# Kernel optimization log

Hardware: AMD Instinct MI355X
Metric: run time of the kernel (lower is better)

The kernel has to match this reference:

```python
import jax, jax.numpy as jnp
import numpy as np

DIM = 768
NUM_HEADS = 12
POLY_DEG = 3
GRID = (24, 24)
BATCH = 16


def _make_powers():
    H, W = GRID
    ii, jj = np.meshgrid(np.arange(H), np.arange(W), indexing='ij')
    coords = np.stack([ii.ravel(), jj.ravel()], axis=-1).astype(np.float32)  # [HW, 2]
    dists = np.abs(coords[:, None, :] - coords[None, :, :]).sum(-1)  # L1 cdist [HW, HW]
    powers = np.stack([dists ** i for i in range(POLY_DEG + 1)], axis=0)  # [deg+1, HW, HW]
    return jnp.asarray(powers, dtype=jnp.float32)


def setup_inputs() -> dict:
    key = jax.random.key(0)
    ks = jax.random.split(key, 5)
    N = GRID[0] * GRID[1] + 1  # 577
    x = jax.random.normal(ks[0], (BATCH, N, DIM), dtype=jnp.float32)
    # nn.Linear weights stored as [in, out] for direct matmul; qkv_bias=False
    W_qkv = jax.random.normal(ks[1], (DIM, 3 * DIM), dtype=jnp.float32) * (DIM ** -0.5)
    W_proj = jax.random.normal(ks[2], (DIM, DIM), dtype=jnp.float32) * (DIM ** -0.5)
    b_proj = jnp.zeros((DIM,), dtype=jnp.float32)
    # small scale keeps polynomial bias (distances up to 46, cubed) numerically sane
    poly_coeffs = jax.random.normal(ks[3], (NUM_HEADS, POLY_DEG + 1), dtype=jnp.float32) * 0.01
    powers = _make_powers()
    return {"x": x, "W_qkv": W_qkv, "W_proj": W_proj, "b_proj": b_proj,
            "poly_coeffs": poly_coeffs, "powers": powers}


def reference(x, W_qkv, W_proj, b_proj, poly_coeffs, powers):
    B, N, C = x.shape
    h = NUM_HEADS
    d = C // h
    scale = d ** -0.5
    qkv = (x @ W_qkv).reshape(B, N, 3, h, d)
    qkv = jnp.transpose(qkv, (2, 0, 3, 1, 4))  # [3, B, h, N, d]
    q, k, v = qkv[0], qkv[1], qkv[2]
    # polynomial relative-position bias, padded with zeros for CLS row/col
    rpe = jnp.einsum('hd,dxy->hxy', poly_coeffs, powers)  # [h, HW, HW]
    rpe = jnp.pad(rpe, ((0, 0), (1, 0), (1, 0)))  # [h, N, N]
    attn = scale * jnp.einsum('bhnd,bhmd->bhnm', q, k) + rpe[None]
    attn = jax.nn.softmax(attn, axis=-1)
    out = jnp.einsum('bhnm,bhmd->bhnd', attn, v)
    out = jnp.transpose(out, (0, 2, 1, 3)).reshape(B, N, C)
    return out @ W_proj + b_proj
```

## Files before the change

kernel.cpp:

```cpp
#include <hip/hip_runtime.h>


using u16 = unsigned short;
using u32 = unsigned int;

typedef __bf16 bf16x8 __attribute__((ext_vector_type(8)));
typedef float f32x4 __attribute__((ext_vector_type(4)));

__device__ inline u16 f2bf(float f) {
    u32 u = __builtin_bit_cast(u32, f);
    u32 r = u + 0x7fffu + ((u >> 16) & 1u);
    return (u16)(r >> 16);
}
__device__ inline float bf2f(u16 x) {
    return __builtin_bit_cast(float, (u32)x << 16);
}

__device__ inline f32x4 mfma16(bf16x8 a, bf16x8 b, f32x4 c) {
    return __builtin_amdgcn_mfma_f32_16x16x32_bf16(a, b, c, 0, 0, 0);
}

__device__ inline float fexp2(float x) { return __builtin_amdgcn_exp2f(x); }

__device__ inline int xcd_remap(int bid, int nwg) {
    const int q = nwg >> 3, r = nwg & 7;
    const int xcd = bid & 7, idx = bid >> 3;
    return (xcd < r ? xcd * (q + 1) : r * (q + 1) + (xcd - r) * q) + idx;
}

__device__ inline float dpp_max16(float v) {
    int x;
    x = __builtin_amdgcn_update_dpp(0, __builtin_bit_cast(int, v), 0xB1, 0xF, 0xF, true);
    v = fmaxf(v, __builtin_bit_cast(float, x));
    x = __builtin_amdgcn_update_dpp(0, __builtin_bit_cast(int, v), 0x4E, 0xF, 0xF, true);
    v = fmaxf(v, __builtin_bit_cast(float, x));
    x = __builtin_amdgcn_update_dpp(0, __builtin_bit_cast(int, v), 0x124, 0xF, 0xF, true);
    v = fmaxf(v, __builtin_bit_cast(float, x));
    x = __builtin_amdgcn_update_dpp(0, __builtin_bit_cast(int, v), 0x128, 0xF, 0xF, true);
    v = fmaxf(v, __builtin_bit_cast(float, x));
    return v;
}
__device__ inline float dpp_sum16(float v) {
    int x;
    x = __builtin_amdgcn_update_dpp(0, __builtin_bit_cast(int, v), 0xB1, 0xF, 0xF, true);
    v += __builtin_bit_cast(float, x);
    x = __builtin_amdgcn_update_dpp(0, __builtin_bit_cast(int, v), 0x4E, 0xF, 0xF, true);
    v += __builtin_bit_cast(float, x);
    x = __builtin_amdgcn_update_dpp(0, __builtin_bit_cast(int, v), 0x124, 0xF, 0xF, true);
    v += __builtin_bit_cast(float, x);
    x = __builtin_amdgcn_update_dpp(0, __builtin_bit_cast(int, v), 0x128, 0xF, 0xF, true);
    v += __builtin_bit_cast(float, x);
    return v;
}

#define GLOAD_LDS16(g, l)                                                          \
    __builtin_amdgcn_global_load_lds((const __attribute__((address_space(1))) u32*)(g), \
                                     (__attribute__((address_space(3))) u32*)(l), 16, 0, 0)

#define BAR()    asm volatile("s_barrier" ::: "memory")
#define WAITV8() asm volatile("s_waitcnt vmcnt(8)" ::: "memory")
#define WAITV4() asm volatile("s_waitcnt vmcnt(4)" ::: "memory")
#define WAITV0() asm volatile("s_waitcnt vmcnt(0)" ::: "memory")

__global__ void k_prep(const float* __restrict__ x, const float* __restrict__ Wq,
                       const float* __restrict__ Wp, u16* __restrict__ xb,
                       u16* __restrict__ wqkv, u16* __restrict__ wprj) {
    const int bid = blockIdx.x;
    const int t = threadIdx.x;
    if (bid < 576) {
        __shared__ float tile[64][65];
        const float* src;
        u16* dst;
        int C, rt, ct;
        if (bid < 432) { src = Wq; dst = wqkv; C = 2304; rt = bid / 36; ct = bid % 36; }
        else { const int b2 = bid - 432; src = Wp; dst = wprj; C = 768; rt = b2 / 12; ct = b2 % 12; }
        const int row0 = rt * 64, col0 = ct * 64;
#pragma unroll
        for (int it = 0; it < 4; ++it) {
            const int row = it * 16 + (t >> 4);
            const float4 v = *(const float4*)&src[(size_t)(row0 + row) * C + col0 + (t & 15) * 4];
            tile[row][(t & 15) * 4 + 0] = v.x;
            tile[row][(t & 15) * 4 + 1] = v.y;
            tile[row][(t & 15) * 4 + 2] = v.z;
            tile[row][(t & 15) * 4 + 3] = v.w;
        }
        __syncthreads();
#pragma unroll
        for (int it = 0; it < 4; ++it) {
            const int oc = it * 16 + (t >> 4);
            const int orr = (t & 15) * 4;
            ushort4 o;
            o.x = f2bf(tile[orr + 0][oc]);
            o.y = f2bf(tile[orr + 1][oc]);
            o.z = f2bf(tile[orr + 2][oc]);
            o.w = f2bf(tile[orr + 3][oc]);
            *(ushort4*)&dst[(size_t)(col0 + oc) * 768 + row0 + orr] = o;
        }
    } else {
        const int n4 = 9232 * 768 / 4;
        const int stride = (2048 - 576) * 256;
        for (int i = (bid - 576) * 256 + t; i < n4; i += stride) {
            float4 v = ((const float4*)x)[i];
            ushort4 o;
            o.x = f2bf(v.x); o.y = f2bf(v.y); o.z = f2bf(v.z); o.w = f2bf(v.w);
            ((ushort4*)xb)[i] = o;
        }
    }
}

__device__ inline void stageAB(const u16* __restrict__ Ag, const u16* __restrict__ Bg,
                               u16* L, int t) {
#pragma unroll
    for (int c = 0; c < 2; ++c) {
        const int p = c * 256 + t;
        const int row = p >> 2, ch = p & 3;
        const int src = row * 768 + ((ch ^ ((row >> 1) & 3)) * 8);
        GLOAD_LDS16(Ag + src, L + p * 8);
        GLOAD_LDS16(Bg + src, L + 4096 + p * 8);
    }
}
__device__ inline bf16x8 ldfrag32(const u16* base, int row, int slot) {
    return *(const bf16x8*)(base + row * 32 + ((slot ^ ((row >> 1) & 3)) * 8));
}

template <int MODE, int NB>
__launch_bounds__(256, 2)
__global__ void k_gemm(const u16* __restrict__ A, const u16* __restrict__ Bw,
                       u16* __restrict__ q_out, u16* __restrict__ k_out,
                       u16* __restrict__ v_out,
                       float* __restrict__ f_out, const float* __restrict__ bias) {
    constexpr int NT = 24;
    constexpr int M = 9232;
    const int wgid = xcd_remap(blockIdx.x, gridDim.x);
    const int mbase = (wgid / NB) * 128;
    const int nbase = (wgid - (wgid / NB) * NB) * 128;
    __shared__ alignas(16) u16 lds[4][8192];
    const int t = threadIdx.x;
    const int lane = t & 63, w = t >> 6;
    const int lr = lane & 15, lg = lane >> 4;
    const int wrow = (w >> 1) * 64, wcol = (w & 1) * 64;
    const u16* Ag = A + (size_t)mbase * 768;
    const u16* Bg = Bw + (size_t)nbase * 768;
    f32x4 acc[4][4] = {};

    stageAB(Ag, Bg, &lds[0][0], t);
    stageAB(Ag + 32, Bg + 32, &lds[1][0], t);
    stageAB(Ag + 64, Bg + 64, &lds[2][0], t);
    WAITV8();
    BAR();

    for (int kt = 0; kt < NT; ++kt) {
        const u16* Lc = &lds[kt & 3][0];
        if (kt + 3 < NT)
            stageAB(Ag + (kt + 3) * 32, Bg + (kt + 3) * 32, &lds[(kt + 3) & 3][0], t);
        bf16x8 af[4], bv[4];
#pragma unroll
        for (int i = 0; i < 4; ++i)
            af[i] = ldfrag32(Lc, wrow + i * 16 + lr, lg);
#pragma unroll
        for (int j = 0; j < 4; ++j)
            bv[j] = ldfrag32(Lc + 4096, wcol + j * 16 + lr, lg);
        __builtin_amdgcn_s_setprio(1);
#pragma unroll
        for (int i = 0; i < 4; ++i)
#pragma unroll
            for (int j = 0; j < 4; ++j)
                acc[i][j] = mfma16(af[i], bv[j], acc[i][j]);
        __builtin_amdgcn_s_setprio(0);
        if (kt + 1 < NT) {
            if (kt < NT - 3)       { WAITV8(); }
            else if (kt == NT - 3) { WAITV4(); }
            else                   { WAITV0(); }
            BAR();
        }
    }

#pragma unroll
    for (int i = 0; i < 4; ++i) {
#pragma unroll
        for (int j = 0; j < 4; ++j) {
            const int col = nbase + wcol + j * 16 + lr;
#pragma unroll
            for (int r = 0; r < 4; ++r) {
                const int row = mbase + wrow + i * 16 + 4 * lg + r;
                if (row < M) {
                    if (MODE == 0) {
                        const int bb = row / 577;
                        const int nn = row - bb * 577;
                        const int tt = col / 768;
                        const int rem = col - tt * 768;
                        const int hh = rem >> 6, dd = rem & 63;
                        const size_t bh = (size_t)bb * 12 + hh;
                        const u16 val = f2bf(acc[i][j][r]);
                        if (tt == 0)      q_out[(bh * 640 + nn) * 64 + dd] = val;
                        else if (tt == 1) k_out[(bh * 640 + nn) * 64 + dd] = val;
                        else              v_out[(bh * 64 + dd) * 640 + nn] = val;
                    } else {
                        f_out[(size_t)row * 768 + col] = acc[i][j][r] + bias[col];
                    }
                }
            }
        }
    }
}

__launch_bounds__(256, 2)
__global__ void k_attn(const u16* __restrict__ Qg, const u16* __restrict__ Kg,
                       const u16* __restrict__ Vtg, const float* __restrict__ coef,
                       u16* __restrict__ Og) {
    const int wgid = xcd_remap(blockIdx.x, gridDim.x);
    const int bh = wgid / 5;
    const int qt = wgid - bh * 5;
    const int b = bh / 12, h = bh - b * 12;
    const int t = threadIdx.x;
    const int lane = t & 63, w = t >> 6;
    const int lr = lane & 15, lg = lane >> 4;
    __shared__ alignas(16) u16 Kl[2][4096];
    __shared__ alignas(16) u16 Vl[2][4096];

    const float l2e = 1.4426950408889634f;
    const float hc0 = coef[h * 4 + 0] * l2e, hc1 = coef[h * 4 + 1] * l2e,
                hc2 = coef[h * 4 + 2] * l2e, hc3 = coef[h * 4 + 3] * l2e;

    const int qrow0 = qt * 128 + w * 32;
    bf16x8 qa[2][2];
#pragma unroll
    for (int i = 0; i < 2; ++i) {
        const u16* qp = Qg + ((size_t)bh * 640 + qrow0 + i * 16 + lr) * 64;
        qa[i][0] = *(const bf16x8*)(qp + lg * 8);
        qa[i][1] = *(const bf16x8*)(qp + 32 + lg * 8);
    }

    float gi[2][4], gj[2][4], nvf[2][4];
#pragma unroll
    for (int i = 0; i < 2; ++i)
#pragma unroll
        for (int r = 0; r < 4; ++r) {
            const int n = qrow0 + i * 16 + 4 * lg + r;
            nvf[i][r] = (n == 0) ? 0.f : 1.f;
            const int nm1 = (n > 0) ? n - 1 : 0;
            const int qi = nm1 / 24;
            gi[i][r] = (float)qi;
            gj[i][r] = (float)(nm1 - qi * 24);
        }

    float M[2][4], L[2][4];
#pragma unroll
    for (int i = 0; i < 2; ++i)
#pragma unroll
        for (int r = 0; r < 4; ++r) { M[i][r] = -3e38f; L[i][r] = 0.f; }
    f32x4 acco[2][4] = {};
    const float scale2 = 0.125f * 1.4426950408889634f;
    const int ch0 = ((lg ^ (lr & 7))) * 8;

    const u16* Ksb = Kg + (size_t)bh * 640 * 64;
    const u16* Vsb = Vtg + (size_t)bh * 64 * 640;
    const int sr0 = lane >> 3, sc = lane & 7;
    const int kr0 = 16 * w + sr0, kr1 = kr0 + 8;
    const int kd0 = kr0 * 64 + ((sc ^ (kr0 & 7)) * 8);
    const int kd1 = kr1 * 64 + ((sc ^ (kr1 & 7)) * 8);

    {
        uint4 k0 = *(const uint4*)(Ksb + kr0 * 64 + sc * 8);
        uint4 k1 = *(const uint4*)(Ksb + kr1 * 64 + sc * 8);
        uint4 v0 = *(const uint4*)(Vsb + (size_t)kr0 * 640 + sc * 8);
        uint4 v1 = *(const uint4*)(Vsb + (size_t)kr1 * 640 + sc * 8);
        *(uint4*)(&Kl[0][kd0]) = k0;
        *(uint4*)(&Kl[0][kd1]) = k1;
        *(uint4*)(&Vl[0][kd0]) = v0;
        *(uint4*)(&Vl[0][kd1]) = v1;
    }
    __syncthreads();
    int cur = 0;

    for (int kt = 0; kt < 9; ++kt) {
        const u16* Kc = &Kl[cur][0];
        const u16* Vc = &Vl[cur][0];
        u16* pb0 = &Kl[cur ^ 1][16 * w * 64];
        u16* pb1 = &Vl[cur ^ 1][16 * w * 64];

        f32x4 sac[2][4];
        __builtin_amdgcn_s_setprio(1);
#pragma unroll
        for (int cb = 0; cb < 4; ++cb) {
            const int row = cb * 16 + lr;
            const bf16x8 kb0 = *(const bf16x8*)(Kc + row * 64 + ch0);
            const bf16x8 kb1 = *(const bf16x8*)(Kc + row * 64 + (ch0 ^ 32));
#pragma unroll
            for (int i = 0; i < 2; ++i) {
                f32x4 z = {};
                z = mfma16(qa[i][0], kb0, z);
                sac[i][cb] = mfma16(qa[i][1], kb1, z);
            }
        }
        __builtin_amdgcn_s_setprio(0);

        float tm[2][4];
#pragma unroll
        for (int i = 0; i < 2; ++i)
#pragma unroll
            for (int r = 0; r < 4; ++r) tm[i][r] = -3e38f;
#pragma unroll
        for (int cb = 0; cb < 4; ++cb) {
            const int m = kt * 64 + cb * 16 + lr;
            const float mvf = (m == 0) ? 0.f : 1.f;
            const int mm1 = (m > 0) ? m - 1 : 0;
            const int pi = mm1 / 24;
            const float ci = (float)pi;
            const float cj = (float)(mm1 - pi * 24);
#pragma unroll
            for (int i = 0; i < 2; ++i)
#pragma unroll
                for (int r = 0; r < 4; ++r) {
                    const float d = fabsf(gi[i][r] - ci) + fabsf(gj[i][r] - cj);
                    float rp = fmaf(hc3, d, hc2);
                    rp = fmaf(rp, d, hc1);
                    rp = fmaf(rp, d, hc0);
                    const float v = fmaf(sac[i][cb][r], scale2,
                                         rp * (mvf * nvf[i][r]));
                    sac[i][cb][r] = v;
                    tm[i][r] = fmaxf(tm[i][r], v);
                }
        }
#pragma unroll
        for (int i = 0; i < 2; ++i)
#pragma unroll
            for (int r = 0; r < 4; ++r) tm[i][r] = dpp_max16(tm[i][r]);

        float over = -3e38f;
#pragma unroll
        for (int i = 0; i < 2; ++i)
#pragma unroll
            for (int r = 0; r < 4; ++r) over = fmaxf(over, tm[i][r] - M[i][r]);
        if (__any(over > 11.5f)) {
#pragma unroll
            for (int i = 0; i < 2; ++i)
#pragma unroll
                for (int r = 0; r < 4; ++r) {
                    const float Mn = fmaxf(M[i][r], tm[i][r]);
                    const float a = fexp2(M[i][r] - Mn);
                    L[i][r] *= a;
                    acco[i][0][r] *= a; acco[i][1][r] *= a;
                    acco[i][2][r] *= a; acco[i][3][r] *= a;
                    M[i][r] = Mn;
                }
        }

#pragma unroll
        for (int i = 0; i < 2; ++i) {
            u16* pb = i ? pb1 : pb0;
#pragma unroll
            for (int cb = 0; cb < 4; ++cb)
#pragma unroll
                for (int r = 0; r < 4; ++r) {
                    const float p = fexp2(sac[i][cb][r] - M[i][r]);
                    L[i][r] += p;
                    const int rw = 4 * lg + r;
                    pb[rw * 64 + (((2 * cb + (lr >> 3)) ^ (rw & 7)) * 8) + (lr & 7)] = f2bf(p);
                }
        }

        uint4 nk0, nk1, nv0, nv1;
        {
            const u16* Ks = Ksb + (size_t)(kt + 1) * 64 * 64;
            const u16* Vs = Vsb + (size_t)(kt + 1) * 64;
            nk0 = *(const uint4*)(Ks + kr0 * 64 + sc * 8);
            nk1 = *(const uint4*)(Ks + kr1 * 64 + sc * 8);
            nv0 = *(const uint4*)(Vs + (size_t)kr0 * 640 + sc * 8);
            nv1 = *(const uint4*)(Vs + (size_t)kr1 * 640 + sc * 8);
        }

        const bf16x8 pa00 = *(const bf16x8*)(pb0 + lr * 64 + ch0);
        const bf16x8 pa01 = *(const bf16x8*)(pb0 + lr * 64 + (ch0 ^ 32));
        const bf16x8 pa10 = *(const bf16x8*)(pb1 + lr * 64 + ch0);
        const bf16x8 pa11 = *(const bf16x8*)(pb1 + lr * 64 + (ch0 ^ 32));
        __builtin_amdgcn_s_setprio(1);
#pragma unroll
        for (int f = 0; f < 4; ++f) {
            const int vrow = f * 16 + lr;
            const bf16x8 vb0 = *(const bf16x8*)(Vc + vrow * 64 + ch0);
            const bf16x8 vb1 = *(const bf16x8*)(Vc + vrow * 64 + (ch0 ^ 32));
            acco[0][f] = mfma16(pa00, vb0, acco[0][f]);
            acco[0][f] = mfma16(pa01, vb1, acco[0][f]);
            acco[1][f] = mfma16(pa10, vb0, acco[1][f]);
            acco[1][f] = mfma16(pa11, vb1, acco[1][f]);
        }
        __builtin_amdgcn_s_setprio(0);

        *(uint4*)(&Kl[cur ^ 1][kd0]) = nk0;
        *(uint4*)(&Kl[cur ^ 1][kd1]) = nk1;
        *(uint4*)(&Vl[cur ^ 1][kd0]) = nv0;
        *(uint4*)(&Vl[cur ^ 1][kd1]) = nv1;
        __syncthreads();
        cur ^= 1;
    }

    {
        const u16* Kc = &Kl[cur][0];
        const u16* Vc = &Vl[cur][0];
        u16* pb0 = &Kl[cur ^ 1][16 * w * 64];
        u16* pb1 = &Vl[cur ^ 1][16 * w * 64];
        const bf16x8 kb0 = *(const bf16x8*)(Kc + lr * 64 + ch0);
        const bf16x8 kb1 = *(const bf16x8*)(Kc + lr * 64 + (ch0 ^ 32));
        float s0[2][4], tm[2][4];
#pragma unroll
        for (int i = 0; i < 2; ++i) {
            f32x4 z = {};
            z = mfma16(qa[i][0], kb0, z);
            const f32x4 sc0 = mfma16(qa[i][1], kb1, z);
#pragma unroll
            for (int r = 0; r < 4; ++r) {
                const float d = fabsf(gi[i][r] - 23.f) + fabsf(gj[i][r] - 23.f);
                float rp = fmaf(hc3, d, hc2);
                rp = fmaf(rp, d, hc1);
                rp = fmaf(rp, d, hc0);
                float v = fmaf(sc0[r], scale2, rp * nvf[i][r]);
                v = (lr == 0) ? v : -1e30f;
                s0[i][r] = v;
                tm[i][r] = dpp_max16(v);
            }
        }
        float over = -3e38f;
#pragma unroll
        for (int i = 0; i < 2; ++i)
#pragma unroll
            for (int r = 0; r < 4; ++r) over = fmaxf(over, tm[i][r] - M[i][r]);
        if (__any(over > 11.5f)) {
#pragma unroll
            for (int i = 0; i < 2; ++i)
#pragma unroll
                for (int r = 0; r < 4; ++r) {
                    const float Mn = fmaxf(M[i][r], tm[i][r]);
                    const float a = fexp2(M[i][r] - Mn);
                    L[i][r] *= a;
                    acco[i][0][r] *= a; acco[i][1][r] *= a;
                    acco[i][2][r] *= a; acco[i][3][r] *= a;
                    M[i][r] = Mn;
                }
        }
#pragma unroll
        for (int i = 0; i < 2; ++i) {
            u16* pb = i ? pb1 : pb0;
#pragma unroll
            for (int cb = 0; cb < 4; ++cb)
#pragma unroll
                for (int r = 0; r < 4; ++r) {
                    const float p = (cb == 0) ? fexp2(s0[i][r] - M[i][r]) : 0.f;
                    L[i][r] += p;
                    const int rw = 4 * lg + r;
                    pb[rw * 64 + (((2 * cb + (lr >> 3)) ^ (rw & 7)) * 8) + (lr & 7)] = f2bf(p);
                }
        }
        const bf16x8 pa00 = *(const bf16x8*)(pb0 + lr * 64 + ch0);
        const bf16x8 pa10 = *(const bf16x8*)(pb1 + lr * 64 + ch0);
#pragma unroll
        for (int f = 0; f < 4; ++f) {
            const int vrow = f * 16 + lr;
            const bf16x8 vb0 = *(const bf16x8*)(Vc + vrow * 64 + ch0);
            acco[0][f] = mfma16(pa00, vb0, acco[0][f]);
            acco[1][f] = mfma16(pa10, vb0, acco[1][f]);
        }
    }

#pragma unroll
    for (int i = 0; i < 2; ++i)
#pragma unroll
        for (int r = 0; r < 4; ++r) {
            const float inv = __builtin_amdgcn_rcpf(dpp_sum16(L[i][r]));
            const int n = qrow0 + i * 16 + 4 * lg + r;
            if (n < 577) {
#pragma unroll
                for (int f = 0; f < 4; ++f)
                    Og[((size_t)b * 577 + n) * 768 + h * 64 + f * 16 + lr] =
                        f2bf(acco[i][f][r] * inv);
            }
        }
}

extern "C" void kernel_launch(void* const* d_in, const int* in_sizes, int n_in,
                              void* d_out, int out_size, void* d_ws, size_t ws_size,
                              hipStream_t stream) {
    const float* x      = (const float*)d_in[0];
    const float* W_qkv  = (const float*)d_in[1];
    const float* W_proj = (const float*)d_in[2];
    const float* b_proj = (const float*)d_in[3];
    const float* coef   = (const float*)d_in[4];
    float* out = (float*)d_out;
    char* ws = (char*)d_ws;

    u16* xb   = (u16*)(ws + 0);
    u16* Og   = (u16*)(ws + 0);
    u16* wqkv = (u16*)(ws + 14180352);
    u16* wprj = (u16*)(ws + 17719296);
    u16* Qg   = (u16*)(ws + 18898944);
    u16* Kg   = (u16*)(ws + 34627584);
    u16* Vtg  = (u16*)(ws + 50356224);

    k_prep<<<2048, 256, 0, stream>>>(x, W_qkv, W_proj, xb, wqkv, wprj);

    k_gemm<0, 18><<<18 * 73, 256, 0, stream>>>(xb, wqkv, Qg, Kg, Vtg,
                                               nullptr, nullptr);
    k_attn<<<960, 256, 0, stream>>>(Qg, Kg, Vtg, coef, Og);
    k_gemm<1, 6><<<6 * 73, 256, 0, stream>>>(Og, wprj, nullptr, nullptr,
                                             nullptr, out, b_proj);
}
```

Measured before the change: 166.3 us.

## Widen GEMM N-tile to 192 and switch to triple-buffered LDS pipeline

The GEMM tile width along N becomes a template parameter: both the QKV and output projections now use 128x192 tiles, with each wave covering 96 columns. The LDS ring drops from four stages with prefetch distance 3 to three stages with prefetch distance 2, and the vmcnt waits are adjusted to match. The wider tile cuts the number of workgroups and the redundant reloads of A, which raises data reuse. In exchange it uses more accumulator registers per wave and hides less global-load latency with the shallower prefetch.

```diff
diff --git a/kernel.cpp b/kernel.cpp
--- a/kernel.cpp
+++ b/kernel.cpp
@@ -58,8 +58,7 @@
                                      (__attribute__((address_space(3))) u32*)(l), 16, 0, 0)
 
 #define BAR()    asm volatile("s_barrier" ::: "memory")
-#define WAITV8() asm volatile("s_waitcnt vmcnt(8)" ::: "memory")
-#define WAITV4() asm volatile("s_waitcnt vmcnt(4)" ::: "memory")
+#define WAITV5() asm volatile("s_waitcnt vmcnt(5)" ::: "memory")
 #define WAITV0() asm volatile("s_waitcnt vmcnt(0)" ::: "memory")
 
 __global__ void k_prep(const float* __restrict__ x, const float* __restrict__ Wq,
@@ -108,22 +107,28 @@
     }
 }
 
+template <int NJ>
 __device__ inline void stageAB(const u16* __restrict__ Ag, const u16* __restrict__ Bg,
                                u16* L, int t) {
 #pragma unroll
     for (int c = 0; c < 2; ++c) {
         const int p = c * 256 + t;
         const int row = p >> 2, ch = p & 3;
-        const int src = row * 768 + ((ch ^ ((row >> 1) & 3)) * 8);
-        GLOAD_LDS16(Ag + src, L + p * 8);
-        GLOAD_LDS16(Bg + src, L + 4096 + p * 8);
+        GLOAD_LDS16(Ag + row * 768 + ((ch ^ ((row >> 1) & 3)) * 8), L + p * 8);
+    }
+#pragma unroll
+    for (int c = 0; c < NJ / 2; ++c) {
+        const int p = c * 256 + t;
+        const int row = p >> 2, ch = p & 3;
+        GLOAD_LDS16(Bg + row * 768 + ((ch ^ ((row >> 1) & 3)) * 8),
+                    L + 4096 + p * 8);
     }
 }
 __device__ inline bf16x8 ldfrag32(const u16* base, int row, int slot) {
     return *(const bf16x8*)(base + row * 32 + ((slot ^ ((row >> 1) & 3)) * 8));
 }
 
-template <int MODE, int NB>
+template <int MODE, int NB, int NJ>
 __launch_bounds__(256, 2)
 __global__ void k_gemm(const u16* __restrict__ A, const u16* __restrict__ Bw,
                        u16* __restrict__ q_out, u16* __restrict__ k_out,
@@ -131,46 +136,46 @@
                        float* __restrict__ f_out, const float* __restrict__ bias) {
     constexpr int NT = 24;
     constexpr int M = 9232;
+    constexpr int BN = NJ * 32;
     const int wgid = xcd_remap(blockIdx.x, gridDim.x);
     const int mbase = (wgid / NB) * 128;
-    const int nbase = (wgid - (wgid / NB) * NB) * 128;
-    __shared__ alignas(16) u16 lds[4][8192];
+    const int nbase = (wgid - (wgid / NB) * NB) * BN;
+    __shared__ alignas(16) u16 lds[3][4096 + NJ * 1024];
     const int t = threadIdx.x;
     const int lane = t & 63, w = t >> 6;
     const int lr = lane & 15, lg = lane >> 4;
-    const int wrow = (w >> 1) * 64, wcol = (w & 1) * 64;
+    const int wrow = (w >> 1) * 64, wcol = (w & 1) * (NJ * 16);
     const u16* Ag = A + (size_t)mbase * 768;
     const u16* Bg = Bw + (size_t)nbase * 768;
-    f32x4 acc[4][4] = {};
-
-    stageAB(Ag, Bg, &lds[0][0], t);
-    stageAB(Ag + 32, Bg + 32, &lds[1][0], t);
-    stageAB(Ag + 64, Bg + 64, &lds[2][0], t);
-    WAITV8();
+    f32x4 acc[4][NJ] = {};
+
+    stageAB<NJ>(Ag, Bg, &lds[0][0], t);
+    stageAB<NJ>(Ag + 32, Bg + 32, &lds[1][0], t);
+    WAITV5();
     BAR();
 
     for (int kt = 0; kt < NT; ++kt) {
-        const u16* Lc = &lds[kt & 3][0];
-        if (kt + 3 < NT)
-            stageAB(Ag + (kt + 3) * 32, Bg + (kt + 3) * 32, &lds[(kt + 3) & 3][0], t);
-        bf16x8 af[4], bv[4];
+        const u16* Lc = &lds[kt % 3][0];
+        const bool m2 = (kt + 2) < NT;
+        if (m2)
+            stageAB<NJ>(Ag + (kt + 2) * 32, Bg + (kt + 2) * 32,
+                        &lds[(kt + 2) % 3][0], t);
+        bf16x8 af[4], bv[NJ];
 #pragma unroll
         for (int i = 0; i < 4; ++i)
             af[i] = ldfrag32(Lc, wrow + i * 16 + lr, lg);
 #pragma unroll
-        for (int j = 0; j < 4; ++j)
+        for (int j = 0; j < NJ; ++j)
             bv[j] = ldfrag32(Lc + 4096, wcol + j * 16 + lr, lg);
         __builtin_amdgcn_s_setprio(1);
 #pragma unroll
         for (int i = 0; i < 4; ++i)
 #pragma unroll
-            for (int j = 0; j < 4; ++j)
+            for (int j = 0; j < NJ; ++j)
                 acc[i][j] = mfma16(af[i], bv[j], acc[i][j]);
         __builtin_amdgcn_s_setprio(0);
         if (kt + 1 < NT) {
-            if (kt < NT - 3)       { WAITV8(); }
-            else if (kt == NT - 3) { WAITV4(); }
-            else                   { WAITV0(); }
+            if (m2) { WAITV5(); } else { WAITV0(); }
             BAR();
         }
     }
@@ -178,7 +183,7 @@
 #pragma unroll
     for (int i = 0; i < 4; ++i) {
 #pragma unroll
-        for (int j = 0; j < 4; ++j) {
+        for (int j = 0; j < NJ; ++j) {
             const int col = nbase + wcol + j * 16 + lr;
 #pragma unroll
             for (int r = 0; r < 4; ++r) {
@@ -498,9 +503,9 @@
 
     k_prep<<<2048, 256, 0, stream>>>(x, W_qkv, W_proj, xb, wqkv, wprj);
 
-    k_gemm<0, 18><<<18 * 73, 256, 0, stream>>>(xb, wqkv, Qg, Kg, Vtg,
-                                               nullptr, nullptr);
+    k_gemm<0, 12, 6><<<12 * 73, 256, 0, stream>>>(xb, wqkv, Qg, Kg, Vtg,
+                                                  nullptr, nullptr);
     k_attn<<<960, 256, 0, stream>>>(Qg, Kg, Vtg, coef, Og);
-    k_gemm<1, 6><<<6 * 73, 256, 0, stream>>>(Og, wprj, nullptr, nullptr,
-                                             nullptr, out, b_proj);
-}
+    k_gemm<1, 4, 6><<<4 * 73, 256, 0, stream>>>(Og, wprj, nullptr, nullptr,
+                                                nullptr, out, b_proj);
+}
```

Result: slower. 172.9 us (+4.0%).

## Double attention KV tile width to 128 keys per iteration

Applied to the files above, without the earlier changes.

Switches the flash-attention loop from 64-key tiles (9 full iterations plus a tail) to 128-key tiles (4 full iterations plus an 80-key tail). The goal is fewer loop trips and barriers, with more MFMA and exp work between synchronizations. To support this, the K/V loading layout, the LDS swizzle (16-chunk XOR for V and the P buffer) and the P·V inner loop are restructured. LDS usage doubles to 64KB, which may limit occupancy against the 2-block launch bound, and register pressure grows with sac[2][8].

```diff
diff --git a/kernel.cpp b/kernel.cpp
--- a/kernel.cpp
+++ b/kernel.cpp
@@ -215,8 +215,8 @@
     const int t = threadIdx.x;
     const int lane = t & 63, w = t >> 6;
     const int lr = lane & 15, lg = lane >> 4;
-    __shared__ alignas(16) u16 Kl[2][4096];
-    __shared__ alignas(16) u16 Vl[2][4096];
+    __shared__ alignas(16) u16 Kl[2][8192];
+    __shared__ alignas(16) u16 Vl[2][8192];
 
     const float l2e = 1.4426950408889634f;
     const float hc0 = coef[h * 4 + 0] * l2e, hc1 = coef[h * 4 + 1] * l2e,
@@ -255,34 +255,31 @@
 
     const u16* Ksb = Kg + (size_t)bh * 640 * 64;
     const u16* Vsb = Vtg + (size_t)bh * 64 * 640;
-    const int sr0 = lane >> 3, sc = lane & 7;
-    const int kr0 = 16 * w + sr0, kr1 = kr0 + 8;
-    const int kd0 = kr0 * 64 + ((sc ^ (kr0 & 7)) * 8);
-    const int kd1 = kr1 * 64 + ((sc ^ (kr1 & 7)) * 8);
+    const int krow = 32 * w + (lane >> 1), kch0 = (lane & 1) * 4;
+    const int vrow = 16 * w + (lane >> 2), vch0 = (lane & 3) * 4;
 
     {
-        uint4 k0 = *(const uint4*)(Ksb + kr0 * 64 + sc * 8);
-        uint4 k1 = *(const uint4*)(Ksb + kr1 * 64 + sc * 8);
-        uint4 v0 = *(const uint4*)(Vsb + (size_t)kr0 * 640 + sc * 8);
-        uint4 v1 = *(const uint4*)(Vsb + (size_t)kr1 * 640 + sc * 8);
-        *(uint4*)(&Kl[0][kd0]) = k0;
-        *(uint4*)(&Kl[0][kd1]) = k1;
-        *(uint4*)(&Vl[0][kd0]) = v0;
-        *(uint4*)(&Vl[0][kd1]) = v1;
+#pragma unroll
+        for (int q = 0; q < 4; ++q) {
+            uint4 kv = *(const uint4*)(Ksb + (size_t)krow * 64 + (kch0 + q) * 8);
+            *(uint4*)(&Kl[0][krow * 64 + (((kch0 + q) ^ (krow & 7)) * 8)]) = kv;
+            uint4 vv = *(const uint4*)(Vsb + (size_t)vrow * 640 + (vch0 + q) * 8);
+            *(uint4*)(&Vl[0][vrow * 128 + (((vch0 + q) ^ (vrow & 15)) * 8)]) = vv;
+        }
     }
     __syncthreads();
     int cur = 0;
 
-    for (int kt = 0; kt < 9; ++kt) {
+    for (int kt = 0; kt < 4; ++kt) {
         const u16* Kc = &Kl[cur][0];
         const u16* Vc = &Vl[cur][0];
-        u16* pb0 = &Kl[cur ^ 1][16 * w * 64];
-        u16* pb1 = &Vl[cur ^ 1][16 * w * 64];
-
-        f32x4 sac[2][4];
+        u16* pb0 = &Kl[cur ^ 1][32 * w * 64];
+        u16* pb1 = &Vl[cur ^ 1][16 * w * 128];
+
+        f32x4 sac[2][8];
         __builtin_amdgcn_s_setprio(1);
 #pragma unroll
-        for (int cb = 0; cb < 4; ++cb) {
+        for (int cb = 0; cb < 8; ++cb) {
             const int row = cb * 16 + lr;
             const bf16x8 kb0 = *(const bf16x8*)(Kc + row * 64 + ch0);
             const bf16x8 kb1 = *(const bf16x8*)(Kc + row * 64 + (ch0 ^ 32));
@@ -301,8 +298,8 @@
 #pragma unroll
             for (int r = 0; r < 4; ++r) tm[i][r] = -3e38f;
 #pragma unroll
-        for (int cb = 0; cb < 4; ++cb) {
-            const int m = kt * 64 + cb * 16 + lr;
+        for (int cb = 0; cb < 8; ++cb) {
+            const int m = kt * 128 + cb * 16 + lr;
             const float mvf = (m == 0) ? 0.f : 1.f;
             const int mm1 = (m > 0) ? m - 1 : 0;
             const int pi = mm1 / 24;
@@ -350,47 +347,47 @@
         for (int i = 0; i < 2; ++i) {
             u16* pb = i ? pb1 : pb0;
 #pragma unroll
-            for (int cb = 0; cb < 4; ++cb)
+            for (int cb = 0; cb < 8; ++cb)
 #pragma unroll
                 for (int r = 0; r < 4; ++r) {
                     const float p = fexp2(sac[i][cb][r] - M[i][r]);
                     L[i][r] += p;
                     const int rw = 4 * lg + r;
-                    pb[rw * 64 + (((2 * cb + (lr >> 3)) ^ (rw & 7)) * 8) + (lr & 7)] = f2bf(p);
-                }
-        }
-
-        uint4 nk0, nk1, nv0, nv1;
+                    pb[rw * 128 + (((2 * cb + (lr >> 3)) ^ (rw & 15)) * 8) + (lr & 7)] = f2bf(p);
+                }
+        }
+
+        uint4 nk[4], nv[4];
         {
-            const u16* Ks = Ksb + (size_t)(kt + 1) * 64 * 64;
-            const u16* Vs = Vsb + (size_t)(kt + 1) * 64;
-            nk0 = *(const uint4*)(Ks + kr0 * 64 + sc * 8);
-            nk1 = *(const uint4*)(Ks + kr1 * 64 + sc * 8);
-            nv0 = *(const uint4*)(Vs + (size_t)kr0 * 640 + sc * 8);
-            nv1 = *(const uint4*)(Vs + (size_t)kr1 * 640 + sc * 8);
-        }
-
-        const bf16x8 pa00 = *(const bf16x8*)(pb0 + lr * 64 + ch0);
-        const bf16x8 pa01 = *(const bf16x8*)(pb0 + lr * 64 + (ch0 ^ 32));
-        const bf16x8 pa10 = *(const bf16x8*)(pb1 + lr * 64 + ch0);
-        const bf16x8 pa11 = *(const bf16x8*)(pb1 + lr * 64 + (ch0 ^ 32));
+            const u16* Ks = Ksb + (size_t)(kt + 1) * 128 * 64;
+            const u16* Vs = Vsb + (size_t)(kt + 1) * 128;
+#pragma unroll
+            for (int q = 0; q < 4; ++q) {
+                nk[q] = *(const uint4*)(Ks + (size_t)krow * 64 + (kch0 + q) * 8);
+                nv[q] = *(const uint4*)(Vs + (size_t)vrow * 640 + (vch0 + q) * 8);
+            }
+        }
+
         __builtin_amdgcn_s_setprio(1);
 #pragma unroll
-        for (int f = 0; f < 4; ++f) {
-            const int vrow = f * 16 + lr;
-            const bf16x8 vb0 = *(const bf16x8*)(Vc + vrow * 64 + ch0);
-            const bf16x8 vb1 = *(const bf16x8*)(Vc + vrow * 64 + (ch0 ^ 32));
-            acco[0][f] = mfma16(pa00, vb0, acco[0][f]);
-            acco[0][f] = mfma16(pa01, vb1, acco[0][f]);
-            acco[1][f] = mfma16(pa10, vb0, acco[1][f]);
-            acco[1][f] = mfma16(pa11, vb1, acco[1][f]);
+        for (int s = 0; s < 4; ++s) {
+            const bf16x8 pa0 = *(const bf16x8*)(pb0 + lr * 128 + (((4 * s + lg) ^ (lr & 15)) * 8));
+            const bf16x8 pa1 = *(const bf16x8*)(pb1 + lr * 128 + (((4 * s + lg) ^ (lr & 15)) * 8));
+#pragma unroll
+            for (int f = 0; f < 4; ++f) {
+                const int vr = f * 16 + lr;
+                const bf16x8 vb = *(const bf16x8*)(Vc + vr * 128 + (((4 * s + lg) ^ (vr & 15)) * 8));
+                acco[0][f] = mfma16(pa0, vb, acco[0][f]);
+                acco[1][f] = mfma16(pa1, vb, acco[1][f]);
+            }
         }
         __builtin_amdgcn_s_setprio(0);
 
-        *(uint4*)(&Kl[cur ^ 1][kd0]) = nk0;
-        *(uint4*)(&Kl[cur ^ 1][kd1]) = nk1;
-        *(uint4*)(&Vl[cur ^ 1][kd0]) = nv0;
-        *(uint4*)(&Vl[cur ^ 1][kd1]) = nv1;
+#pragma unroll
+        for (int q = 0; q < 4; ++q) {
+            *(uint4*)(&Kl[cur ^ 1][krow * 64 + (((kch0 + q) ^ (krow & 7)) * 8)]) = nk[q];
+            *(uint4*)(&Vl[cur ^ 1][vrow * 128 + (((vch0 + q) ^ (vrow & 15)) * 8)]) = nv[q];
+        }
         __syncthreads();
         cur ^= 1;
     }
@@ -398,28 +395,57 @@
     {
         const u16* Kc = &Kl[cur][0];
         const u16* Vc = &Vl[cur][0];
-        u16* pb0 = &Kl[cur ^ 1][16 * w * 64];
-        u16* pb1 = &Vl[cur ^ 1][16 * w * 64];
-        const bf16x8 kb0 = *(const bf16x8*)(Kc + lr * 64 + ch0);
-        const bf16x8 kb1 = *(const bf16x8*)(Kc + lr * 64 + (ch0 ^ 32));
-        float s0[2][4], tm[2][4];
-#pragma unroll
-        for (int i = 0; i < 2; ++i) {
-            f32x4 z = {};
-            z = mfma16(qa[i][0], kb0, z);
-            const f32x4 sc0 = mfma16(qa[i][1], kb1, z);
-#pragma unroll
-            for (int r = 0; r < 4; ++r) {
-                const float d = fabsf(gi[i][r] - 23.f) + fabsf(gj[i][r] - 23.f);
-                float rp = fmaf(hc3, d, hc2);
-                rp = fmaf(rp, d, hc1);
-                rp = fmaf(rp, d, hc0);
-                float v = fmaf(sc0[r], scale2, rp * nvf[i][r]);
-                v = (lr == 0) ? v : -1e30f;
-                s0[i][r] = v;
-                tm[i][r] = dpp_max16(v);
-            }
-        }
+        u16* pb0 = &Kl[cur ^ 1][32 * w * 64];
+        u16* pb1 = &Vl[cur ^ 1][16 * w * 128];
+
+        f32x4 sac[2][5];
+        __builtin_amdgcn_s_setprio(1);
+#pragma unroll
+        for (int cb = 0; cb < 5; ++cb) {
+            const int row = cb * 16 + lr;
+            const bf16x8 kb0 = *(const bf16x8*)(Kc + row * 64 + ch0);
+            const bf16x8 kb1 = *(const bf16x8*)(Kc + row * 64 + (ch0 ^ 32));
+#pragma unroll
+            for (int i = 0; i < 2; ++i) {
+                f32x4 z = {};
+                z = mfma16(qa[i][0], kb0, z);
+                sac[i][cb] = mfma16(qa[i][1], kb1, z);
+            }
+        }
+        __builtin_amdgcn_s_setprio(0);
+
+        float tm[2][4];
+#pragma unroll
+        for (int i = 0; i < 2; ++i)
+#pragma unroll
+            for (int r = 0; r < 4; ++r) tm[i][r] = -3e38f;
+#pragma unroll
+        for (int cb = 0; cb < 5; ++cb) {
+            const int m = 512 + cb * 16 + lr;
+            const bool valid = (m <= 576);
+            const int mm1 = m - 1;
+            const int pi = mm1 / 24;
+            const float ci = (float)((pi < 24) ? pi : 23);
+            const float cj = (float)((pi < 24) ? (mm1 - pi * 24) : 23);
+#pragma unroll
+            for (int i = 0; i < 2; ++i)
+#pragma unroll
+                for (int r = 0; r < 4; ++r) {
+                    const float d = fabsf(gi[i][r] - ci) + fabsf(gj[i][r] - cj);
+                    float rp = fmaf(hc3, d, hc2);
+                    rp = fmaf(rp, d, hc1);
+                    rp = fmaf(rp, d, hc0);
+                    float v = fmaf(sac[i][cb][r], scale2, rp * nvf[i][r]);
+                    v = valid ? v : -1e30f;
+                    sac[i][cb][r] = v;
+                    tm[i][r] = fmaxf(tm[i][r], v);
+                }
+        }
+#pragma unroll
+        for (int i = 0; i < 2; ++i)
+#pragma unroll
+            for (int r = 0; r < 4; ++r) tm[i][r] = dpp_max16(tm[i][r]);
+
         float over = -3e38f;
 #pragma unroll
         for (int i = 0; i < 2; ++i)
@@ -438,28 +464,40 @@
                     M[i][r] = Mn;
                 }
         }
+
 #pragma unroll
         for (int i = 0; i < 2; ++i) {
             u16* pb = i ? pb1 : pb0;
 #pragma unroll
-            for (int cb = 0; cb < 4; ++cb)
+            for (int cb = 0; cb < 5; ++cb)
 #pragma unroll
                 for (int r = 0; r < 4; ++r) {
-                    const float p = (cb == 0) ? fexp2(s0[i][r] - M[i][r]) : 0.f;
+                    const float p = fexp2(sac[i][cb][r] - M[i][r]);
                     L[i][r] += p;
                     const int rw = 4 * lg + r;
-                    pb[rw * 64 + (((2 * cb + (lr >> 3)) ^ (rw & 7)) * 8) + (lr & 7)] = f2bf(p);
-                }
-        }
-        const bf16x8 pa00 = *(const bf16x8*)(pb0 + lr * 64 + ch0);
-        const bf16x8 pa10 = *(const bf16x8*)(pb1 + lr * 64 + ch0);
-#pragma unroll
-        for (int f = 0; f < 4; ++f) {
-            const int vrow = f * 16 + lr;
-            const bf16x8 vb0 = *(const bf16x8*)(Vc + vrow * 64 + ch0);
-            acco[0][f] = mfma16(pa00, vb0, acco[0][f]);
-            acco[1][f] = mfma16(pa10, vb0, acco[1][f]);
-        }
+                    pb[rw * 128 + (((2 * cb + (lr >> 3)) ^ (rw & 15)) * 8) + (lr & 7)] = f2bf(p);
+                }
+#pragma unroll
+            for (int r = 0; r < 4; ++r) {
+                const int rw = 4 * lg + r;
+                pb[rw * 128 + (((10 + (lr >> 3)) ^ (rw & 15)) * 8) + (lr & 7)] = 0;
+            }
+        }
+
+        __builtin_amdgcn_s_setprio(1);
+#pragma unroll
+        for (int s = 0; s < 3; ++s) {
+            const bf16x8 pa0 = *(const bf16x8*)(pb0 + lr * 128 + (((4 * s + lg) ^ (lr & 15)) * 8));
+            const bf16x8 pa1 = *(const bf16x8*)(pb1 + lr * 128 + (((4 * s + lg) ^ (lr & 15)) * 8));
+#pragma unroll
+            for (int f = 0; f < 4; ++f) {
+                const int vr = f * 16 + lr;
+                const bf16x8 vb = *(const bf16x8*)(Vc + vr * 128 + (((4 * s + lg) ^ (vr & 15)) * 8));
+                acco[0][f] = mfma16(pa0, vb, acco[0][f]);
+                acco[1][f] = mfma16(pa1, vb, acco[1][f]);
+            }
+        }
+        __builtin_amdgcn_s_setprio(0);
     }
 
 #pragma unroll
```

Result: faster. 161.4 us (-2.9%).
